# Kernel tuning notes

Measured on AMD Instinct MI355X. Metric: run time of the kernel, lower is better.

The kernel has to match this reference:

```python
import jax, jax.numpy as jnp
import numpy as np
import math

B, T, DIM, NH, H, K = 8, 1024, 512, 8, 127, 32
HD = DIM // NH
EPS = 1e-5

def _ln(x, g, b):
    m = jnp.mean(x, -1, keepdims=True)
    v = jnp.mean((x - m) ** 2, -1, keepdims=True)
    return (x - m) * jax.lax.rsqrt(v + EPS) * g + b

def _mask_fill(x, mask):
    return jnp.where(mask[..., None], 0.0, x)

def _ffn(x, mask, ng, nb, w1, b1, w2, b2):
    h = _ln(x, ng, nb)
    h = jax.nn.silu(h @ w1 + b1) @ w2 + b2
    return _mask_fill(x + 0.5 * h, mask)

def _mha(x, mask, ng, nb, wqkv, wout, bout, rel_pos):
    b, t, d = x.shape
    h = _ln(x, ng, nb)
    qkv = h @ wqkv                                   # [b,t,3d]
    q, k, v = jnp.split(qkv, 3, axis=-1)
    rs = lambda z: z.reshape(b, t, NH, HD).transpose(0, 2, 1, 3)  # [b,h,t,hd]
    q, k, v = rs(q), rs(k), rs(v)
    scale = 1.0 / math.sqrt(HD)
    scores = jnp.einsum('bhqd,bhkd->bhqk', q, k) * scale
    # relative-position bias: gather per (q,key) offset from [H+1,h,hd] table
    pos = jnp.arange(t)
    rel = jnp.clip(pos[:, None] - pos[None, :], 0, H)            # [t,t] = clamp(q - key)
    qr = jnp.einsum('bhqd,phd->bhqp', q, rel_pos) * scale        # [b,h,t,H+1]
    rel_scores = jnp.take_along_axis(qr, rel[None, None], axis=-1)
    scores = scores + rel_scores
    # causal + horizon mask: allow 0 <= q - key <= H
    diff = pos[:, None] - pos[None, :]
    bad = (diff < 0) | (diff > H)
    scores = jnp.where(bad[None, None], -jnp.inf, scores)
    # key padding
    scores = jnp.where(mask[:, None, None, :], -jnp.inf, scores)
    v = jnp.where(mask[:, None, :, None], 0.0, v)
    attn = jax.nn.softmax(scores, axis=-1)
    out = jnp.einsum('bhqk,bhkd->bhqd', attn, v)
    out = out.transpose(0, 2, 1, 3).reshape(b, t, d)
    out = out @ wout + bout
    return _mask_fill(x + out, mask)

def _conv(x, mask, ng, nb, pw1_w, pw1_b, dw_w, dw_b, bn_g, bn_b, bn_m, bn_v, pw2_w, pw2_b):
    b, t, d = x.shape
    h = _ln(x, ng, nb)
    h = h @ pw1_w + pw1_b                            # [b,t,2d]
    a, g = jnp.split(h, 2, axis=-1)
    h = a * jax.nn.sigmoid(g)                        # GLU
    # causal depthwise conv along time
    hc = h.transpose(0, 2, 1)                        # [b,d,t]
    hc = jnp.pad(hc, ((0, 0), (0, 0), (K - 1, 0)))
    hc = jax.lax.conv_general_dilated(
        hc, dw_w[:, None, :], window_strides=(1,), padding='VALID',
        feature_group_count=d, dimension_numbers=('NCH', 'OIH', 'NCH'))
    hc = hc + dw_b[None, :, None]
    # BatchNorm1d (eval mode, running stats)
    hc = (hc - bn_m[None, :, None]) * jax.lax.rsqrt(bn_v[None, :, None] + EPS)
    hc = hc * bn_g[None, :, None] + bn_b[None, :, None]
    hc = jax.nn.silu(hc)
    h = hc.transpose(0, 2, 1) @ pw2_w + pw2_b
    return _mask_fill(x + h, mask)

def _block(x, mask, p):
    x = _ffn(x, mask, p['ff1_ng'], p['ff1_nb'], p['ff1_w1'], p['ff1_b1'], p['ff1_w2'], p['ff1_b2'])
    x = _mha(x, mask, p['mha_ng'], p['mha_nb'], p['wqkv'], p['wout'], p['bout'], p['rel_pos'])
    x = _conv(x, mask, p['conv_ng'], p['conv_nb'], p['pw1_w'], p['pw1_b'], p['dw_w'], p['dw_b'],
              p['bn_g'], p['bn_b'], p['bn_m'], p['bn_v'], p['pw2_w'], p['pw2_b'])
    x = _ffn(x, mask, p['ff2_ng'], p['ff2_nb'], p['ff2_w1'], p['ff2_b1'], p['ff2_w2'], p['ff2_b2'])
    x = _ln(x, p['final_ng'], p['final_nb'])
    return _mask_fill(x, mask)

def setup_inputs() -> dict:
    key = jax.random.key(0)
    ks = jax.random.split(key, 16)
    s = 0.02
    d = {
        'x': jax.random.normal(ks[0], (B, T, DIM), jnp.float32),
        'mask': jnp.zeros((B, T), bool),
        'ff1_ng': jnp.ones((DIM,)), 'ff1_nb': jnp.zeros((DIM,)),
        'ff1_w1': jax.random.normal(ks[1], (DIM, 4 * DIM)) * s, 'ff1_b1': jnp.zeros((4 * DIM,)),
        'ff1_w2': jax.random.normal(ks[2], (4 * DIM, DIM)) * s, 'ff1_b2': jnp.zeros((DIM,)),
        'mha_ng': jnp.ones((DIM,)), 'mha_nb': jnp.zeros((DIM,)),
        'wqkv': jax.random.normal(ks[3], (DIM, 3 * DIM)) * s,
        'wout': jax.random.normal(ks[4], (DIM, DIM)) * s, 'bout': jnp.zeros((DIM,)),
        'rel_pos': jax.random.normal(ks[5], (H + 1, NH, HD)),
        'conv_ng': jnp.ones((DIM,)), 'conv_nb': jnp.zeros((DIM,)),
        'pw1_w': jax.random.normal(ks[6], (DIM, 2 * DIM)) * s, 'pw1_b': jnp.zeros((2 * DIM,)),
        'dw_w': jax.random.normal(ks[7], (DIM, K)) * s, 'dw_b': jnp.zeros((DIM,)),
        'bn_g': jnp.ones((DIM,)), 'bn_b': jnp.zeros((DIM,)),
        'bn_m': jnp.zeros((DIM,)), 'bn_v': jnp.ones((DIM,)),
        'pw2_w': jax.random.normal(ks[8], (DIM, DIM)) * s, 'pw2_b': jnp.zeros((DIM,)),
        'ff2_ng': jnp.ones((DIM,)), 'ff2_nb': jnp.zeros((DIM,)),
        'ff2_w1': jax.random.normal(ks[9], (DIM, 4 * DIM)) * s, 'ff2_b1': jnp.zeros((4 * DIM,)),
        'ff2_w2': jax.random.normal(ks[10], (4 * DIM, DIM)) * s, 'ff2_b2': jnp.zeros((DIM,)),
        'final_ng': jnp.ones((DIM,)), 'final_nb': jnp.zeros((DIM,)),
    }
    return d

def reference(x, mask, ff1_ng, ff1_nb, ff1_w1, ff1_b1, ff1_w2, ff1_b2,
              mha_ng, mha_nb, wqkv, wout, bout, rel_pos,
              conv_ng, conv_nb, pw1_w, pw1_b, dw_w, dw_b, bn_g, bn_b, bn_m, bn_v, pw2_w, pw2_b,
              ff2_ng, ff2_nb, ff2_w1, ff2_b1, ff2_w2, ff2_b2, final_ng, final_nb):
    p = dict(ff1_ng=ff1_ng, ff1_nb=ff1_nb, ff1_w1=ff1_w1, ff1_b1=ff1_b1, ff1_w2=ff1_w2, ff1_b2=ff1_b2,
             mha_ng=mha_ng, mha_nb=mha_nb, wqkv=wqkv, wout=wout, bout=bout, rel_pos=rel_pos,
             conv_ng=conv_ng, conv_nb=conv_nb, pw1_w=pw1_w, pw1_b=pw1_b, dw_w=dw_w, dw_b=dw_b,
             bn_g=bn_g, bn_b=bn_b, bn_m=bn_m, bn_v=bn_v, pw2_w=pw2_w, pw2_b=pw2_b,
             ff2_ng=ff2_ng, ff2_nb=ff2_nb, ff2_w1=ff2_w1, ff2_b1=ff2_b1, ff2_w2=ff2_w2, ff2_b2=ff2_b2,
             final_ng=final_ng, final_nb=final_nb)
    return _block(x, mask, p)
```

## Files before the change

### kernel.cpp

```cpp
#include <hip/hip_runtime.h>

constexpr int cB = 8, cT = 1024, cD = 512, cNH = 8, cHD = 64, cH = 127, cK = 32;
constexpr int cM = cB * cT;
constexpr float cEPS = 1e-5f;

typedef __attribute__((ext_vector_type(8))) short bf16x8;
typedef __attribute__((ext_vector_type(4))) float f32x4;
typedef __attribute__((ext_vector_type(8))) unsigned short u16x8;

__device__ __forceinline__ float sigm_(float x) { return 1.0f / (1.0f + __expf(-x)); }

__device__ __forceinline__ unsigned short f2bf(float f) {
  union { float f; unsigned int u; } v; v.f = f;
  unsigned int r = v.u + 0x7fffu + ((v.u >> 16) & 1u);
  return (unsigned short)(r >> 16);
}

__device__ __forceinline__ void gload_lds16(const void* g, void* l) {
  __builtin_amdgcn_global_load_lds(
      (const __attribute__((address_space(1))) void*)g,
      (__attribute__((address_space(3))) void*)l, 16, 0, 0);
}

template<bool MASKOUT, bool OUTBF>
__global__ __launch_bounds__(256) void ln_kernel(
    const float* __restrict__ in, const float* __restrict__ gw,
    const float* __restrict__ bw, const unsigned char* __restrict__ mask,
    void* __restrict__ outv) {
  int row = blockIdx.x * 4 + (threadIdx.x >> 6);
  int lane = threadIdx.x & 63;
  const float4* x4 = reinterpret_cast<const float4*>(in + (size_t)row * cD);
  float4 v0 = x4[2 * lane];
  float4 v1 = x4[2 * lane + 1];
  float s = v0.x + v0.y + v0.z + v0.w + v1.x + v1.y + v1.z + v1.w;
  float q = v0.x * v0.x + v0.y * v0.y + v0.z * v0.z + v0.w * v0.w +
            v1.x * v1.x + v1.y * v1.y + v1.z * v1.z + v1.w * v1.w;
#pragma unroll
  for (int m = 1; m < 64; m <<= 1) {
    s += __shfl_xor(s, m);
    q += __shfl_xor(q, m);
  }
  float mean = s * (1.0f / cD);
  float var = q * (1.0f / cD) - mean * mean;
  float rs = rsqrtf(var + cEPS);
  float keep = 1.0f;
  if (MASKOUT) keep = mask[row] ? 0.0f : 1.0f;
  const float4* g4 = reinterpret_cast<const float4*>(gw);
  const float4* b4 = reinterpret_cast<const float4*>(bw);
  float4 ga = g4[2 * lane], gb = g4[2 * lane + 1];
  float4 ba = b4[2 * lane], bb = b4[2 * lane + 1];
  float o[8];
  o[0] = ((v0.x - mean) * rs * ga.x + ba.x) * keep;
  o[1] = ((v0.y - mean) * rs * ga.y + ba.y) * keep;
  o[2] = ((v0.z - mean) * rs * ga.z + ba.z) * keep;
  o[3] = ((v0.w - mean) * rs * ga.w + ba.w) * keep;
  o[4] = ((v1.x - mean) * rs * gb.x + bb.x) * keep;
  o[5] = ((v1.y - mean) * rs * gb.y + bb.y) * keep;
  o[6] = ((v1.z - mean) * rs * gb.z + bb.z) * keep;
  o[7] = ((v1.w - mean) * rs * gb.w + bb.w) * keep;
  if (OUTBF) {
    u16x8 p;
#pragma unroll
    for (int i = 0; i < 8; ++i) p[i] = f2bf(o[i]);
    *reinterpret_cast<u16x8*>((unsigned short*)outv + (size_t)row * cD + lane * 8) = p;
  } else {
    float4 o0 = {o[0], o[1], o[2], o[3]}, o1 = {o[4], o[5], o[6], o[7]};
    float4* o4 = reinterpret_cast<float4*>((float*)outv + (size_t)row * cD);
    o4[2 * lane] = o0;
    o4[2 * lane + 1] = o1;
  }
}

__global__ __launch_bounds__(256) void wconv_kernel(
    const float* __restrict__ W, unsigned short* __restrict__ WT, int K, int N) {
  __shared__ float t[64][65];
  const int n0 = blockIdx.x * 64, k0 = blockIdx.y * 64;
  const int tx = threadIdx.x & 63, ty = threadIdx.x >> 6;
#pragma unroll
  for (int i = 0; i < 16; ++i) {
    int kr = ty * 16 + i;
    t[kr][tx] = W[(size_t)(k0 + kr) * N + n0 + tx];
  }
  __syncthreads();
#pragma unroll
  for (int i = 0; i < 16; ++i) {
    int nr = ty * 16 + i;
    WT[(size_t)(n0 + nr) * K + k0 + tx] = f2bf(t[tx][nr]);
  }
}

__global__ __launch_bounds__(256) void relconv_kernel(
    const float* __restrict__ rel, unsigned short* __restrict__ relT) {
  int flat = (blockIdx.x * 256 + threadIdx.x) * 4;
  int h = flat >> 13, rem = flat & 8191;
  int p = rem >> 6, d = rem & 63;
  float4 v = *reinterpret_cast<const float4*>(rel + ((size_t)p * cNH + h) * cHD + d);
  ushort4 o = {f2bf(v.x), f2bf(v.y), f2bf(v.z), f2bf(v.w)};
  *reinterpret_cast<ushort4*>(relT + flat) = o;
}

template<bool BIAS, bool SILU, int RES, bool MASK, bool OUTBF>
__global__ __launch_bounds__(256) void mgemm_kernel(
    const unsigned short* __restrict__ A, const unsigned short* __restrict__ WT,
    const float* __restrict__ bias, const float* __restrict__ res,
    const unsigned char* __restrict__ mask, void* __restrict__ outv,
    int N, int K) {
  __shared__ unsigned short ldsA[4096];
  __shared__ unsigned short ldsB[4096];
  const int tid = threadIdx.x, lane = tid & 63, wid = tid >> 6;
  const int m0 = blockIdx.y * 128, n0 = blockIdx.x * 128;
  const int wr = wid >> 1, wc = wid & 1;

  const int sr = wid * 32 + (lane >> 2);
  const int sc = (lane & 3) * 8;
  const unsigned short* a0 = A + (size_t)(m0 + sr) * K + sc;
  const unsigned short* a1 = A + (size_t)(m0 + sr + 16) * K + sc;
  const unsigned short* b0 = WT + (size_t)(n0 + sr) * K + sc;
  const unsigned short* b1 = WT + (size_t)(n0 + sr + 16) * K + sc;
  unsigned short* lA0 = ldsA + wid * 1024;
  unsigned short* lA1 = lA0 + 512;
  unsigned short* lB0 = ldsB + wid * 1024;
  unsigned short* lB1 = lB0 + 512;

  f32x4 acc[4][4] = {};

  const int fr = lane & 15, fq = lane >> 4;
  const int fco = fq * 8;

  for (int k0 = 0; k0 < K; k0 += 32) {
    __syncthreads();
    gload_lds16(a0 + k0, lA0);
    gload_lds16(a1 + k0, lA1);
    gload_lds16(b0 + k0, lB0);
    gload_lds16(b1 + k0, lB1);
    asm volatile("s_waitcnt vmcnt(0)" ::: "memory");
    __syncthreads();
    bf16x8 af[4], bfr[4];
#pragma unroll
    for (int f = 0; f < 4; ++f) {
      af[f] = *reinterpret_cast<const bf16x8*>(ldsA + (wr * 64 + f * 16 + fr) * 32 + fco);
      bfr[f] = *reinterpret_cast<const bf16x8*>(ldsB + (wc * 64 + f * 16 + fr) * 32 + fco);
    }
#pragma unroll
    for (int i = 0; i < 4; ++i)
#pragma unroll
      for (int j = 0; j < 4; ++j)
        acc[i][j] = __builtin_amdgcn_mfma_f32_16x16x32_bf16(af[i], bfr[j], acc[i][j], 0, 0, 0);
  }

#pragma unroll
  for (int fm = 0; fm < 4; ++fm) {
#pragma unroll
    for (int fn = 0; fn < 4; ++fn) {
      const int cn = n0 + wc * 64 + fn * 16 + fr;
      const float bv = BIAS ? bias[cn] : 0.0f;
#pragma unroll
      for (int j = 0; j < 4; ++j) {
        const int m = m0 + wr * 64 + fm * 16 + fq * 4 + j;
        float t = acc[fm][fn][j] + bv;
        if (SILU) t = t * sigm_(t);
        if (RES == 1) t = res[(size_t)m * N + cn] + t;
        if (RES == 2) t = res[(size_t)m * N + cn] + 0.5f * t;
        if (MASK) t = mask[m] ? 0.0f : t;
        if (OUTBF) ((unsigned short*)outv)[(size_t)m * N + cn] = f2bf(t);
        else       ((float*)outv)[(size_t)m * N + cn] = t;
      }
    }
  }
}

__global__ __launch_bounds__(128) void attn_kernel(
    const unsigned short* __restrict__ qkv, const unsigned short* __restrict__ relT,
    const unsigned char* __restrict__ mask, unsigned short* __restrict__ out) {
  __shared__ alignas(16) unsigned short Kb[160 * 72];
  __shared__ alignas(16) unsigned short VTs[64 * 160];
  __shared__ alignas(16) char uni[2][8448];
  __shared__ unsigned char msk[160];
  const int tid = threadIdx.x;
  const int b = blockIdx.z, h = blockIdx.y, q0 = blockIdx.x * 32;

  for (int s = tid; s < 160; s += 128) {
    int t = q0 - 127 + s;
    msk[s] = (t < 0 || t >= cT) ? 1 : mask[(size_t)b * cT + t];
  }
  for (int i = tid; i < 1280; i += 128) {
    int row = i >> 3, ch = i & 7;
    int t = q0 - 127 + row;
    bf16x8 v = {};
    if (t >= 0 && t < cT)
      v = *reinterpret_cast<const bf16x8*>(qkv + (size_t)(b * cT + t) * 1536 + 512 + h * 64 + ch * 8);
    *reinterpret_cast<bf16x8*>(Kb + row * 72 + ch * 8) = v;
  }
  for (int i = tid; i < 1280; i += 128) {
    int row = i >> 3, ch = i & 7;
    int t = q0 - 127 + row;
    u16x8 v = {};
    if (t >= 0 && t < cT)
      v = *reinterpret_cast<const u16x8*>(qkv + (size_t)(b * cT + t) * 1536 + 1024 + h * 64 + ch * 8);
#pragma unroll
    for (int e = 0; e < 8; ++e) VTs[(ch * 8 + e) * 160 + row] = v[e];
  }
  __syncthreads();

  const int w = tid >> 6, lane = tid & 63;
  const int fr = lane & 15, fq = lane >> 4;

  const unsigned short* qp = qkv + (size_t)(b * cT + q0 + w * 16 + fr) * 1536 + h * 64;
  bf16x8 qf0 = *reinterpret_cast<const bf16x8*>(qp + fq * 8);
  bf16x8 qf1 = *reinterpret_cast<const bf16x8*>(qp + 32 + fq * 8);

  f32x4 sacc[10] = {};
#pragma unroll
  for (int f = 0; f < 10; ++f) {
    const unsigned short* kb = Kb + (f * 16 + fr) * 72;
    sacc[f] = __builtin_amdgcn_mfma_f32_16x16x32_bf16(qf0, *reinterpret_cast<const bf16x8*>(kb + fq * 8), sacc[f], 0, 0, 0);
    sacc[f] = __builtin_amdgcn_mfma_f32_16x16x32_bf16(qf1, *reinterpret_cast<const bf16x8*>(kb + 32 + fq * 8), sacc[f], 0, 0, 0);
  }
  f32x4 qr[8] = {};
  const unsigned short* rT = relT + (size_t)h * 8192;
#pragma unroll
  for (int fp = 0; fp < 8; ++fp) {
    const unsigned short* rb = rT + (fp * 16 + fr) * 64;
    qr[fp] = __builtin_amdgcn_mfma_f32_16x16x32_bf16(qf0, *reinterpret_cast<const bf16x8*>(rb + fq * 8), qr[fp], 0, 0, 0);
    qr[fp] = __builtin_amdgcn_mfma_f32_16x16x32_bf16(qf1, *reinterpret_cast<const bf16x8*>(rb + 32 + fq * 8), qr[fp], 0, 0, 0);
  }
  float* QR = reinterpret_cast<float*>(uni[w]);
#pragma unroll
  for (int fp = 0; fp < 8; ++fp)
#pragma unroll
    for (int j = 0; j < 4; ++j)
      QR[(fq * 4 + j) * 132 + fp * 16 + fr] = qr[fp][j];
  asm volatile("s_waitcnt lgkmcnt(0)" ::: "memory");
  __builtin_amdgcn_sched_barrier(0);

  float pmat[10][4];
  float mrow[4] = {-3e38f, -3e38f, -3e38f, -3e38f};
#pragma unroll
  for (int f = 0; f < 10; ++f) {
    int slot = f * 16 + fr;
#pragma unroll
    for (int j = 0; j < 4; ++j) {
      int row = fq * 4 + j;
      int pidx = w * 16 + row + 127 - slot;
      float v = -1e30f;
      if ((unsigned)pidx <= 127u && !msk[slot])
        v = (sacc[f][j] + QR[row * 132 + pidx]) * 0.125f;
      pmat[f][j] = v;
      mrow[j] = fmaxf(mrow[j], v);
    }
  }
#pragma unroll
  for (int j = 0; j < 4; ++j) {
    float m = mrow[j];
    m = fmaxf(m, __shfl_xor(m, 1));
    m = fmaxf(m, __shfl_xor(m, 2));
    m = fmaxf(m, __shfl_xor(m, 4));
    m = fmaxf(m, __shfl_xor(m, 8));
    mrow[j] = m;
  }
  float srow[4] = {0.f, 0.f, 0.f, 0.f};
#pragma unroll
  for (int f = 0; f < 10; ++f)
#pragma unroll
    for (int j = 0; j < 4; ++j) {
      float p = __expf(pmat[f][j] - mrow[j]);
      pmat[f][j] = p;
      srow[j] += p;
    }
#pragma unroll
  for (int j = 0; j < 4; ++j) {
    float s = srow[j];
    s += __shfl_xor(s, 1);
    s += __shfl_xor(s, 2);
    s += __shfl_xor(s, 4);
    s += __shfl_xor(s, 8);
    srow[j] = 1.0f / s;
  }
  unsigned short* P = reinterpret_cast<unsigned short*>(uni[w]);
#pragma unroll
  for (int f = 0; f < 10; ++f)
#pragma unroll
    for (int j = 0; j < 4; ++j)
      P[(fq * 4 + j) * 168 + f * 16 + fr] = f2bf(pmat[f][j] * srow[j]);
  asm volatile("s_waitcnt lgkmcnt(0)" ::: "memory");
  __builtin_amdgcn_sched_barrier(0);

  f32x4 oacc[4] = {};
#pragma unroll
  for (int ks = 0; ks < 5; ++ks) {
    bf16x8 pa = *reinterpret_cast<const bf16x8*>(P + fr * 168 + ks * 32 + fq * 8);
#pragma unroll
    for (int fn = 0; fn < 4; ++fn)
      oacc[fn] = __builtin_amdgcn_mfma_f32_16x16x32_bf16(
          pa, *reinterpret_cast<const bf16x8*>(VTs + (fn * 16 + fr) * 160 + ks * 32 + fq * 8), oacc[fn], 0, 0, 0);
  }
#pragma unroll
  for (int fn = 0; fn < 4; ++fn)
#pragma unroll
    for (int j = 0; j < 4; ++j)
      out[(size_t)(b * cT + q0 + w * 16 + fq * 4 + j) * cD + h * 64 + fn * 16 + fr] = f2bf(oacc[fn][j]);
}

__global__ __launch_bounds__(256) void dwconv_kernel(
    const float* __restrict__ pw1out, const float* __restrict__ dww,
    const float* __restrict__ dwb, const float* __restrict__ bng,
    const float* __restrict__ bnb, const float* __restrict__ bnm,
    const float* __restrict__ bnv, unsigned short* __restrict__ out) {
  constexpr int TT = 64, DD = 128, PAD = cK - 1;
  __shared__ alignas(16) float g_lds[TT + PAD][DD];
  const int b = blockIdx.z, d0 = blockIdx.y * DD, t0 = blockIdx.x * TT;
  const int tid = threadIdx.x;

  for (int f = tid; f < (TT + PAD) * (DD / 4); f += 256) {
    int row = f >> 5, c4 = (f & 31) * 4;
    int t = t0 - PAD + row;
    float4 val = {0.f, 0.f, 0.f, 0.f};
    if (t >= 0) {
      const float* base = pw1out + (size_t)(b * cT + t) * (2 * cD) + d0 + c4;
      float4 a = *reinterpret_cast<const float4*>(base);
      float4 g = *reinterpret_cast<const float4*>(base + cD);
      val.x = a.x * sigm_(g.x);
      val.y = a.y * sigm_(g.y);
      val.z = a.z * sigm_(g.z);
      val.w = a.w * sigm_(g.w);
    }
    *reinterpret_cast<float4*>(&g_lds[row][c4]) = val;
  }
  __syncthreads();

  const int dl = tid & 127, tg = tid >> 7;
  const int d = d0 + dl;
  float w[cK];
  const float4* w4 = reinterpret_cast<const float4*>(dww + (size_t)d * cK);
#pragma unroll
  for (int i = 0; i < cK / 4; ++i) {
    float4 t4 = w4[i];
    w[i * 4 + 0] = t4.x; w[i * 4 + 1] = t4.y; w[i * 4 + 2] = t4.z; w[i * 4 + 3] = t4.w;
  }
  const float bias = dwb[d];
  const float scale = bng[d] * rsqrtf(bnv[d] + cEPS);
  const float shift = bnb[d] - bnm[d] * scale;
#pragma unroll 4
  for (int i = 0; i < 32; ++i) {
    int tl = tg * 32 + i;
    float acc = bias;
#pragma unroll
    for (int k = 0; k < cK; ++k) acc += w[k] * g_lds[tl + k][dl];
    float v = acc * scale + shift;
    v = v * sigm_(v);
    out[(size_t)(b * cT + t0 + tl) * cD + d] = f2bf(v);
  }
}

extern "C" void kernel_launch(void* const* d_in, const int* in_sizes, int n_in,
                              void* d_out, int out_size, void* d_ws, size_t ws_size,
                              hipStream_t stream) {
  const float* x = (const float*)d_in[0];
  const unsigned char* mask = (const unsigned char*)d_in[1];
  const float* ff1_ng = (const float*)d_in[2];
  const float* ff1_nb = (const float*)d_in[3];
  const float* ff1_w1 = (const float*)d_in[4];
  const float* ff1_b1 = (const float*)d_in[5];
  const float* ff1_w2 = (const float*)d_in[6];
  const float* ff1_b2 = (const float*)d_in[7];
  const float* mha_ng = (const float*)d_in[8];
  const float* mha_nb = (const float*)d_in[9];
  const float* wqkv = (const float*)d_in[10];
  const float* wout = (const float*)d_in[11];
  const float* bout = (const float*)d_in[12];
  const float* rel_pos = (const float*)d_in[13];
  const float* conv_ng = (const float*)d_in[14];
  const float* conv_nb = (const float*)d_in[15];
  const float* pw1_w = (const float*)d_in[16];
  const float* pw1_b = (const float*)d_in[17];
  const float* dw_w = (const float*)d_in[18];
  const float* dw_b = (const float*)d_in[19];
  const float* bn_g = (const float*)d_in[20];
  const float* bn_b = (const float*)d_in[21];
  const float* bn_m = (const float*)d_in[22];
  const float* bn_v = (const float*)d_in[23];
  const float* pw2_w = (const float*)d_in[24];
  const float* pw2_b = (const float*)d_in[25];
  const float* ff2_ng = (const float*)d_in[26];
  const float* ff2_nb = (const float*)d_in[27];
  const float* ff2_w1 = (const float*)d_in[28];
  const float* ff2_b1 = (const float*)d_in[29];
  const float* ff2_w2 = (const float*)d_in[30];
  const float* ff2_b2 = (const float*)d_in[31];
  const float* final_ng = (const float*)d_in[32];
  const float* final_nb = (const float*)d_in[33];

  float* X = (float*)d_out;
  char* wsb = (char*)d_ws;
  unsigned short* lnb = (unsigned short*)wsb;
  unsigned short* auxb = (unsigned short*)(wsb + (8 << 20));
  char* big = wsb + (16 << 20);
  unsigned short* wT = (unsigned short*)(wsb + (64 << 20));
  float* bigf = (float*)big;
  unsigned short* bigh = (unsigned short*)big;

  unsigned short* wt_ff1w1 = wT + 0;
  unsigned short* wt_ff1w2 = wT + 1048576;
  unsigned short* wt_qkv   = wT + 2097152;
  unsigned short* wt_out   = wT + 2883584;
  unsigned short* wt_pw1   = wT + 3145728;
  unsigned short* wt_pw2   = wT + 3670016;
  unsigned short* wt_ff2w1 = wT + 3932160;
  unsigned short* wt_ff2w2 = wT + 4980736;
  unsigned short* relT     = wT + 6029312;

  const dim3 blk(256);
  const dim3 ln_grid(cM / 4);

  wconv_kernel<<<dim3(2048 / 64, 512 / 64), blk, 0, stream>>>(ff1_w1, wt_ff1w1, 512, 2048);
  wconv_kernel<<<dim3(512 / 64, 2048 / 64), blk, 0, stream>>>(ff1_w2, wt_ff1w2, 2048, 512);
  wconv_kernel<<<dim3(1536 / 64, 512 / 64), blk, 0, stream>>>(wqkv, wt_qkv, 512, 1536);
  wconv_kernel<<<dim3(512 / 64, 512 / 64), blk, 0, stream>>>(wout, wt_out, 512, 512);
  wconv_kernel<<<dim3(1024 / 64, 512 / 64), blk, 0, stream>>>(pw1_w, wt_pw1, 512, 1024);
  wconv_kernel<<<dim3(512 / 64, 512 / 64), blk, 0, stream>>>(pw2_w, wt_pw2, 512, 512);
  wconv_kernel<<<dim3(2048 / 64, 512 / 64), blk, 0, stream>>>(ff2_w1, wt_ff2w1, 512, 2048);
  wconv_kernel<<<dim3(512 / 64, 2048 / 64), blk, 0, stream>>>(ff2_w2, wt_ff2w2, 2048, 512);
  relconv_kernel<<<dim3(64), blk, 0, stream>>>(rel_pos, relT);

  ln_kernel<false, true><<<ln_grid, blk, 0, stream>>>(x, ff1_ng, ff1_nb, nullptr, lnb);
  mgemm_kernel<true, true, 0, false, true><<<dim3(16, 64), blk, 0, stream>>>(
      lnb, wt_ff1w1, ff1_b1, nullptr, nullptr, bigh, 2048, 512);
  mgemm_kernel<true, false, 2, true, false><<<dim3(4, 64), blk, 0, stream>>>(
      bigh, wt_ff1w2, ff1_b2, x, mask, X, 512, 2048);
  ln_kernel<false, true><<<ln_grid, blk, 0, stream>>>(X, mha_ng, mha_nb, nullptr, lnb);
  mgemm_kernel<false, false, 0, false, true><<<dim3(12, 64), blk, 0, stream>>>(
      lnb, wt_qkv, nullptr, nullptr, nullptr, bigh, 1536, 512);
  attn_kernel<<<dim3(cT / 32, cNH, cB), dim3(128), 0, stream>>>(bigh, relT, mask, auxb);
  mgemm_kernel<true, false, 1, true, false><<<dim3(4, 64), blk, 0, stream>>>(
      auxb, wt_out, bout, X, mask, X, 512, 512);
  ln_kernel<false, true><<<ln_grid, blk, 0, stream>>>(X, conv_ng, conv_nb, nullptr, lnb);
  mgemm_kernel<true, false, 0, false, false><<<dim3(8, 64), blk, 0, stream>>>(
      lnb, wt_pw1, pw1_b, nullptr, nullptr, bigf, 1024, 512);
  dwconv_kernel<<<dim3(cT / 64, cD / 128, cB), blk, 0, stream>>>(
      bigf, dw_w, dw_b, bn_g, bn_b, bn_m, bn_v, auxb);
  mgemm_kernel<true, false, 1, true, false><<<dim3(4, 64), blk, 0, stream>>>(
      auxb, wt_pw2, pw2_b, X, mask, X, 512, 512);
  ln_kernel<false, true><<<ln_grid, blk, 0, stream>>>(X, ff2_ng, ff2_nb, nullptr, lnb);
  mgemm_kernel<true, true, 0, false, true><<<dim3(16, 64), blk, 0, stream>>>(
      lnb, wt_ff2w1, ff2_b1, nullptr, nullptr, bigh, 2048, 512);
  mgemm_kernel<true, false, 2, true, false><<<dim3(4, 64), blk, 0, stream>>>(
      bigh, wt_ff2w2, ff2_b2, X, mask, X, 512, 2048);
  ln_kernel<true, false><<<ln_grid, blk, 0, stream>>>(X, final_ng, final_nb, mask, X);
}
```

Baseline: 520.9 us.

## Double-buffer GEMM LDS, enlarge attention tiles, store pw1 output in bf16

The GEMM main loop now double-buffers its LDS tiles, so the next K-slice's global-to-LDS loads are issued before the MFMAs on the current slice and one barrier per iteration is dropped. The attention kernel moves to 64 queries per 256-thread block and reuses one LDS buffer for K and then V-transpose, which amortizes the halo load over more queries and frees registers. The pw1 GEMM writes bf16 instead of fp32, halving the dwconv input traffic at the cost of extra rounding before the GLU. Doubled LDS per GEMM block may lower occupancy.

```diff
diff --git a/kernel.cpp b/kernel.cpp
--- a/kernel.cpp
+++ b/kernel.cpp
@@ -14,6 +14,10 @@
   union { float f; unsigned int u; } v; v.f = f;
   unsigned int r = v.u + 0x7fffu + ((v.u >> 16) & 1u);
   return (unsigned short)(r >> 16);
+}
+__device__ __forceinline__ float bf2f(unsigned short u) {
+  union { unsigned int u; float f; } v; v.u = (unsigned int)u << 16;
+  return v.f;
 }
 
 __device__ __forceinline__ void gload_lds16(const void* g, void* l) {
@@ -105,8 +109,8 @@
     const float* __restrict__ bias, const float* __restrict__ res,
     const unsigned char* __restrict__ mask, void* __restrict__ outv,
     int N, int K) {
-  __shared__ unsigned short ldsA[4096];
-  __shared__ unsigned short ldsB[4096];
+  __shared__ unsigned short ldsA[2][4096];
+  __shared__ unsigned short ldsB[2][4096];
   const int tid = threadIdx.x, lane = tid & 63, wid = tid >> 6;
   const int m0 = blockIdx.y * 128, n0 = blockIdx.x * 128;
   const int wr = wid >> 1, wc = wid & 1;
@@ -117,35 +121,44 @@
   const unsigned short* a1 = A + (size_t)(m0 + sr + 16) * K + sc;
   const unsigned short* b0 = WT + (size_t)(n0 + sr) * K + sc;
   const unsigned short* b1 = WT + (size_t)(n0 + sr + 16) * K + sc;
-  unsigned short* lA0 = ldsA + wid * 1024;
-  unsigned short* lA1 = lA0 + 512;
-  unsigned short* lB0 = ldsB + wid * 1024;
-  unsigned short* lB1 = lB0 + 512;
+  const int wof = wid * 1024;
 
   f32x4 acc[4][4] = {};
 
   const int fr = lane & 15, fq = lane >> 4;
   const int fco = fq * 8;
 
-  for (int k0 = 0; k0 < K; k0 += 32) {
-    __syncthreads();
-    gload_lds16(a0 + k0, lA0);
-    gload_lds16(a1 + k0, lA1);
-    gload_lds16(b0 + k0, lB0);
-    gload_lds16(b1 + k0, lB1);
+  const int nt = K >> 5;
+  gload_lds16(a0, &ldsA[0][wof]);
+  gload_lds16(a1, &ldsA[0][wof + 512]);
+  gload_lds16(b0, &ldsB[0][wof]);
+  gload_lds16(b1, &ldsB[0][wof + 512]);
+  asm volatile("s_waitcnt vmcnt(0)" ::: "memory");
+  __syncthreads();
+
+  int cur = 0;
+  for (int t = 0; t < nt; ++t) {
+    if (t + 1 < nt) {
+      const int k1 = (t + 1) << 5;
+      gload_lds16(a0 + k1, &ldsA[cur ^ 1][wof]);
+      gload_lds16(a1 + k1, &ldsA[cur ^ 1][wof + 512]);
+      gload_lds16(b0 + k1, &ldsB[cur ^ 1][wof]);
+      gload_lds16(b1 + k1, &ldsB[cur ^ 1][wof + 512]);
+    }
+    bf16x8 af[4], bfr[4];
+#pragma unroll
+    for (int f = 0; f < 4; ++f) {
+      af[f] = *reinterpret_cast<const bf16x8*>(&ldsA[cur][(wr * 64 + f * 16 + fr) * 32 + fco]);
+      bfr[f] = *reinterpret_cast<const bf16x8*>(&ldsB[cur][(wc * 64 + f * 16 + fr) * 32 + fco]);
+    }
+#pragma unroll
+    for (int i = 0; i < 4; ++i)
+#pragma unroll
+      for (int j = 0; j < 4; ++j)
+        acc[i][j] = __builtin_amdgcn_mfma_f32_16x16x32_bf16(af[i], bfr[j], acc[i][j], 0, 0, 0);
     asm volatile("s_waitcnt vmcnt(0)" ::: "memory");
     __syncthreads();
-    bf16x8 af[4], bfr[4];
-#pragma unroll
-    for (int f = 0; f < 4; ++f) {
-      af[f] = *reinterpret_cast<const bf16x8*>(ldsA + (wr * 64 + f * 16 + fr) * 32 + fco);
-      bfr[f] = *reinterpret_cast<const bf16x8*>(ldsB + (wc * 64 + f * 16 + fr) * 32 + fco);
-    }
-#pragma unroll
-    for (int i = 0; i < 4; ++i)
-#pragma unroll
-      for (int j = 0; j < 4; ++j)
-        acc[i][j] = __builtin_amdgcn_mfma_f32_16x16x32_bf16(af[i], bfr[j], acc[i][j], 0, 0, 0);
+    cur ^= 1;
   }
 
 #pragma unroll
@@ -169,36 +182,26 @@
   }
 }
 
-__global__ __launch_bounds__(128) void attn_kernel(
+__global__ __launch_bounds__(256) void attn_kernel(
     const unsigned short* __restrict__ qkv, const unsigned short* __restrict__ relT,
     const unsigned char* __restrict__ mask, unsigned short* __restrict__ out) {
-  __shared__ alignas(16) unsigned short Kb[160 * 72];
-  __shared__ alignas(16) unsigned short VTs[64 * 160];
-  __shared__ alignas(16) char uni[2][8448];
-  __shared__ unsigned char msk[160];
+  __shared__ alignas(16) unsigned short KV[192 * 72];
+  __shared__ alignas(16) float QRu[4][16 * 132];
+  __shared__ unsigned char msk[192];
   const int tid = threadIdx.x;
-  const int b = blockIdx.z, h = blockIdx.y, q0 = blockIdx.x * 32;
-
-  for (int s = tid; s < 160; s += 128) {
+  const int b = blockIdx.z, h = blockIdx.y, q0 = blockIdx.x * 64;
+
+  for (int s = tid; s < 192; s += 256) {
     int t = q0 - 127 + s;
     msk[s] = (t < 0 || t >= cT) ? 1 : mask[(size_t)b * cT + t];
   }
-  for (int i = tid; i < 1280; i += 128) {
+  for (int i = tid; i < 1536; i += 256) {
     int row = i >> 3, ch = i & 7;
     int t = q0 - 127 + row;
     bf16x8 v = {};
     if (t >= 0 && t < cT)
       v = *reinterpret_cast<const bf16x8*>(qkv + (size_t)(b * cT + t) * 1536 + 512 + h * 64 + ch * 8);
-    *reinterpret_cast<bf16x8*>(Kb + row * 72 + ch * 8) = v;
-  }
-  for (int i = tid; i < 1280; i += 128) {
-    int row = i >> 3, ch = i & 7;
-    int t = q0 - 127 + row;
-    u16x8 v = {};
-    if (t >= 0 && t < cT)
-      v = *reinterpret_cast<const u16x8*>(qkv + (size_t)(b * cT + t) * 1536 + 1024 + h * 64 + ch * 8);
-#pragma unroll
-    for (int e = 0; e < 8; ++e) VTs[(ch * 8 + e) * 160 + row] = v[e];
+    *reinterpret_cast<bf16x8*>(KV + row * 72 + ch * 8) = v;
   }
   __syncthreads();
 
@@ -209,10 +212,10 @@
   bf16x8 qf0 = *reinterpret_cast<const bf16x8*>(qp + fq * 8);
   bf16x8 qf1 = *reinterpret_cast<const bf16x8*>(qp + 32 + fq * 8);
 
-  f32x4 sacc[10] = {};
-#pragma unroll
-  for (int f = 0; f < 10; ++f) {
-    const unsigned short* kb = Kb + (f * 16 + fr) * 72;
+  f32x4 sacc[12] = {};
+#pragma unroll
+  for (int f = 0; f < 12; ++f) {
+    const unsigned short* kb = KV + (f * 16 + fr) * 72;
     sacc[f] = __builtin_amdgcn_mfma_f32_16x16x32_bf16(qf0, *reinterpret_cast<const bf16x8*>(kb + fq * 8), sacc[f], 0, 0, 0);
     sacc[f] = __builtin_amdgcn_mfma_f32_16x16x32_bf16(qf1, *reinterpret_cast<const bf16x8*>(kb + 32 + fq * 8), sacc[f], 0, 0, 0);
   }
@@ -224,7 +227,7 @@
     qr[fp] = __builtin_amdgcn_mfma_f32_16x16x32_bf16(qf0, *reinterpret_cast<const bf16x8*>(rb + fq * 8), qr[fp], 0, 0, 0);
     qr[fp] = __builtin_amdgcn_mfma_f32_16x16x32_bf16(qf1, *reinterpret_cast<const bf16x8*>(rb + 32 + fq * 8), qr[fp], 0, 0, 0);
   }
-  float* QR = reinterpret_cast<float*>(uni[w]);
+  float* QR = QRu[w];
 #pragma unroll
   for (int fp = 0; fp < 8; ++fp)
 #pragma unroll
@@ -233,10 +236,9 @@
   asm volatile("s_waitcnt lgkmcnt(0)" ::: "memory");
   __builtin_amdgcn_sched_barrier(0);
 
-  float pmat[10][4];
   float mrow[4] = {-3e38f, -3e38f, -3e38f, -3e38f};
 #pragma unroll
-  for (int f = 0; f < 10; ++f) {
+  for (int f = 0; f < 12; ++f) {
     int slot = f * 16 + fr;
 #pragma unroll
     for (int j = 0; j < 4; ++j) {
@@ -245,7 +247,7 @@
       float v = -1e30f;
       if ((unsigned)pidx <= 127u && !msk[slot])
         v = (sacc[f][j] + QR[row * 132 + pidx]) * 0.125f;
-      pmat[f][j] = v;
+      sacc[f][j] = v;
       mrow[j] = fmaxf(mrow[j], v);
     }
   }
@@ -260,11 +262,11 @@
   }
   float srow[4] = {0.f, 0.f, 0.f, 0.f};
 #pragma unroll
-  for (int f = 0; f < 10; ++f)
+  for (int f = 0; f < 12; ++f)
 #pragma unroll
     for (int j = 0; j < 4; ++j) {
-      float p = __expf(pmat[f][j] - mrow[j]);
-      pmat[f][j] = p;
+      float p = __expf(sacc[f][j] - mrow[j]);
+      sacc[f][j] = p;
       srow[j] += p;
     }
 #pragma unroll
@@ -276,23 +278,37 @@
     s += __shfl_xor(s, 8);
     srow[j] = 1.0f / s;
   }
-  unsigned short* P = reinterpret_cast<unsigned short*>(uni[w]);
-#pragma unroll
-  for (int f = 0; f < 10; ++f)
+  unsigned short* P = reinterpret_cast<unsigned short*>(QRu[w]);
+#pragma unroll
+  for (int f = 0; f < 12; ++f)
 #pragma unroll
     for (int j = 0; j < 4; ++j)
-      P[(fq * 4 + j) * 168 + f * 16 + fr] = f2bf(pmat[f][j] * srow[j]);
-  asm volatile("s_waitcnt lgkmcnt(0)" ::: "memory");
-  __builtin_amdgcn_sched_barrier(0);
+      P[(fq * 4 + j) * 200 + f * 16 + fr] = f2bf(sacc[f][j] * srow[j]);
+
+  __syncthreads();
+  {
+    unsigned short* VT = KV;
+    for (int i = tid; i < 1536; i += 256) {
+      int row = i >> 3, ch = i & 7;
+      int t = q0 - 127 + row;
+      u16x8 v = {};
+      if (t >= 0 && t < cT)
+        v = *reinterpret_cast<const u16x8*>(qkv + (size_t)(b * cT + t) * 1536 + 1024 + h * 64 + ch * 8);
+#pragma unroll
+      for (int e = 0; e < 8; ++e) VT[(ch * 8 + e) * 200 + row] = v[e];
+    }
+  }
+  __syncthreads();
 
   f32x4 oacc[4] = {};
-#pragma unroll
-  for (int ks = 0; ks < 5; ++ks) {
-    bf16x8 pa = *reinterpret_cast<const bf16x8*>(P + fr * 168 + ks * 32 + fq * 8);
+  const unsigned short* VT = KV;
+#pragma unroll
+  for (int ks = 0; ks < 6; ++ks) {
+    bf16x8 pa = *reinterpret_cast<const bf16x8*>(P + fr * 200 + ks * 32 + fq * 8);
 #pragma unroll
     for (int fn = 0; fn < 4; ++fn)
       oacc[fn] = __builtin_amdgcn_mfma_f32_16x16x32_bf16(
-          pa, *reinterpret_cast<const bf16x8*>(VTs + (fn * 16 + fr) * 160 + ks * 32 + fq * 8), oacc[fn], 0, 0, 0);
+          pa, *reinterpret_cast<const bf16x8*>(VT + (fn * 16 + fr) * 200 + ks * 32 + fq * 8), oacc[fn], 0, 0, 0);
   }
 #pragma unroll
   for (int fn = 0; fn < 4; ++fn)
@@ -302,7 +318,7 @@
 }
 
 __global__ __launch_bounds__(256) void dwconv_kernel(
-    const float* __restrict__ pw1out, const float* __restrict__ dww,
+    const unsigned short* __restrict__ pw1out, const float* __restrict__ dww,
     const float* __restrict__ dwb, const float* __restrict__ bng,
     const float* __restrict__ bnb, const float* __restrict__ bnm,
     const float* __restrict__ bnv, unsigned short* __restrict__ out) {
@@ -316,13 +332,13 @@
     int t = t0 - PAD + row;
     float4 val = {0.f, 0.f, 0.f, 0.f};
     if (t >= 0) {
-      const float* base = pw1out + (size_t)(b * cT + t) * (2 * cD) + d0 + c4;
-      float4 a = *reinterpret_cast<const float4*>(base);
-      float4 g = *reinterpret_cast<const float4*>(base + cD);
-      val.x = a.x * sigm_(g.x);
-      val.y = a.y * sigm_(g.y);
-      val.z = a.z * sigm_(g.z);
-      val.w = a.w * sigm_(g.w);
+      const unsigned short* base = pw1out + (size_t)(b * cT + t) * (2 * cD) + d0 + c4;
+      ushort4 a = *reinterpret_cast<const ushort4*>(base);
+      ushort4 g = *reinterpret_cast<const ushort4*>(base + cD);
+      val.x = bf2f(a.x) * sigm_(bf2f(g.x));
+      val.y = bf2f(a.y) * sigm_(bf2f(g.y));
+      val.z = bf2f(a.z) * sigm_(bf2f(g.z));
+      val.w = bf2f(a.w) * sigm_(bf2f(g.w));
     }
     *reinterpret_cast<float4*>(&g_lds[row][c4]) = val;
   }
@@ -396,7 +412,6 @@
   unsigned short* auxb = (unsigned short*)(wsb + (8 << 20));
   char* big = wsb + (16 << 20);
   unsigned short* wT = (unsigned short*)(wsb + (64 << 20));
-  float* bigf = (float*)big;
   unsigned short* bigh = (unsigned short*)big;
 
   unsigned short* wt_ff1w1 = wT + 0;
@@ -430,14 +445,14 @@
   ln_kernel<false, true><<<ln_grid, blk, 0, stream>>>(X, mha_ng, mha_nb, nullptr, lnb);
   mgemm_kernel<false, false, 0, false, true><<<dim3(12, 64), blk, 0, stream>>>(
       lnb, wt_qkv, nullptr, nullptr, nullptr, bigh, 1536, 512);
-  attn_kernel<<<dim3(cT / 32, cNH, cB), dim3(128), 0, stream>>>(bigh, relT, mask, auxb);
+  attn_kernel<<<dim3(cT / 64, cNH, cB), blk, 0, stream>>>(bigh, relT, mask, auxb);
   mgemm_kernel<true, false, 1, true, false><<<dim3(4, 64), blk, 0, stream>>>(
       auxb, wt_out, bout, X, mask, X, 512, 512);
   ln_kernel<false, true><<<ln_grid, blk, 0, stream>>>(X, conv_ng, conv_nb, nullptr, lnb);
-  mgemm_kernel<true, false, 0, false, false><<<dim3(8, 64), blk, 0, stream>>>(
-      lnb, wt_pw1, pw1_b, nullptr, nullptr, bigf, 1024, 512);
+  mgemm_kernel<true, false, 0, false, true><<<dim3(8, 64), blk, 0, stream>>>(
+      lnb, wt_pw1, pw1_b, nullptr, nullptr, bigh, 1024, 512);
   dwconv_kernel<<<dim3(cT / 64, cD / 128, cB), blk, 0, stream>>>(
-      bigf, dw_w, dw_b, bn_g, bn_b, bn_m, bn_v, auxb);
+      bigh, dw_w, dw_b, bn_g, bn_b, bn_m, bn_v, auxb);
   mgemm_kernel<true, false, 1, true, false><<<dim3(4, 64), blk, 0, stream>>>(
       auxb, wt_pw2, pw2_b, X, mask, X, 512, 512);
   ln_kernel<false, true><<<ln_grid, blk, 0, stream>>>(X, ff2_ng, ff2_nb, nullptr, lnb);
```

Measured after the change: 451.4 us. 1.15x faster.
